# Performance work log

Hardware: AMD Instinct MI355X
Metric: run time of the kernel (lower is better)

## Reference

```python
import jax, jax.numpy as jnp
import numpy as np

EMB = 1024
FF = 4096
NE = 8
TOPK = 2
TEMP = 1.0


def setup_inputs() -> dict:
    key = jax.random.key(0)
    ks = jax.random.split(key, 8)
    s_emb = 1.0 / np.sqrt(EMB)
    s_ff = 1.0 / np.sqrt(FF)
    x = jax.random.normal(ks[0], (4, 2048, EMB), dtype=jnp.float32)
    gate_W = jax.random.uniform(ks[1], (EMB, NE), minval=-s_emb, maxval=s_emb, dtype=jnp.float32)
    gate_b = jax.random.uniform(ks[2], (NE,), minval=-s_emb, maxval=s_emb, dtype=jnp.float32)
    W1 = jax.random.uniform(ks[3], (NE, EMB, FF), minval=-s_emb, maxval=s_emb, dtype=jnp.float32)
    b1 = jax.random.uniform(ks[4], (NE, FF), minval=-s_emb, maxval=s_emb, dtype=jnp.float32)
    W2 = jax.random.uniform(ks[5], (NE, FF, EMB), minval=-s_ff, maxval=s_ff, dtype=jnp.float32)
    b2 = jax.random.uniform(ks[6], (NE, EMB), minval=-s_ff, maxval=s_ff, dtype=jnp.float32)
    return {"x": x, "gate_W": gate_W, "gate_b": gate_b, "W1": W1, "b1": b1, "W2": W2, "b2": b2}


def reference(x, gate_W, gate_b, W1, b1, W2, b2):
    B, S, D = x.shape
    xf = x.reshape(-1, D)  # [T, D]
    T = xf.shape[0]

    gate_logits = (xf @ gate_W + gate_b) / TEMP            # [T, E]
    gate_scores = jax.nn.softmax(gate_logits, axis=-1)     # [T, E]
    topk_scores, topk_idx = jax.lax.top_k(gate_scores, TOPK)
    topk_scores = topk_scores / jnp.sum(topk_scores, axis=-1, keepdims=True)

    # combine_weights[t, e] = sum_i topk_scores[t, i] * (topk_idx[t, i] == e)
    onehot = jax.nn.one_hot(topk_idx, NE, dtype=xf.dtype)  # [T, K, E]
    combine = jnp.einsum('tk,tke->te', topk_scores, onehot)  # [T, E]

    # Dense per-expert FFN (dropout is identity in eval): h = gelu(x W1 + b1); y = h W2 + b2
    h = jax.nn.gelu(jnp.einsum('td,edf->etf', xf, W1) + b1[:, None, :], approximate=False)
    y = jnp.einsum('etf,efd->etd', h, W2) + b2[:, None, :]  # [E, T, D]
    out = jnp.einsum('te,etd->td', combine, y).reshape(B, S, D)

    # Load-balance auxiliary loss
    expert_counts = jnp.sum(onehot, axis=(0, 1))            # [E]
    expert_fraction = expert_counts / (T * TOPK)
    routing_weights = jnp.mean(gate_scores, axis=0)
    aux_loss = NE * jnp.sum(expert_fraction * routing_weights)
    return out, aux_loss
```

## Files before the change

kernel.cpp:

```cpp
#include <hip/hip_runtime.h>
#include <math.h>

#define EMB 1024
#define FF  4096
#define NE  8
#define TTOK 8192

typedef __attribute__((ext_vector_type(4))) float  f32x4;
typedef __attribute__((ext_vector_type(8))) __bf16 bf16x8;
typedef __attribute__((ext_vector_type(4))) __bf16 bf16x4;

#define MAXROWS  18432

#define WS_COUNTS  0
#define WS_CURSORS 1024
#define WS_SSUM    2048
#define WS_CELLB   3072
#define WS_NTILES  4096
#define WS_BASE    4100
#define WS_TILE_E  4160
#define WS_TILE_RB 4800
#define WS_TKIDX   8192
#define WS_TKW     73728
#define WS_SLOT    139264
#define WS_TOKID   204800
#define WS_ROWW    278528
#define WS_BIG2    352256

#define SZ_W1T ((size_t)NE * EMB * FF * 2)
#define SZ_W2T ((size_t)NE * EMB * FF * 2)
#define SZ_XB  ((size_t)TTOK * EMB * 2)
#define SZ_H   ((size_t)MAXROWS * FF * 2)
#define SZ_XG  ((size_t)MAXROWS * EMB * 2)
#define SZ_Y2  ((size_t)MAXROWS * EMB * 2)

__device__ inline f32x4 fzero() { f32x4 v = {0.f, 0.f, 0.f, 0.f}; return v; }

__device__ __forceinline__ void gl16(const void* g, void* l) {
    __builtin_amdgcn_global_load_lds(
        (const __attribute__((address_space(1))) void*)g,
        (__attribute__((address_space(3))) void*)l, 16, 0, 0);
}

#define DSR(dst, addr, off) \
    asm volatile("ds_read_b128 %0, %1 offset:" #off : "=v"(dst) : "v"(addr))

__device__ __forceinline__ float gelu_f(float v) {
    float u = fabsf(v) * 0.70710678118654752f;
    float p = 1.0f + u * (0.278393f + u * (0.230389f + u * (0.000972f + u * 0.078108f)));
    p = p * p; p = p * p;
    float er = 1.0f - 1.0f / p;
    float s = (v >= 0.0f) ? er : -er;
    return 0.5f * v * (1.0f + s);
}

__global__ __launch_bounds__(256) void prepass_kernel(
    const float* __restrict__ W1, __bf16* __restrict__ W1T,
    const float* __restrict__ W2, __bf16* __restrict__ W2T,
    const float* __restrict__ x, const float* __restrict__ gW, const float* __restrict__ gb,
    int* counts, float* ssum, int* tk_idx, float* tk_w, __bf16* __restrict__ xb)
{
    __shared__ __bf16 Ls[64 * 72];
    if (blockIdx.x < 16384) {
        int f = blockIdx.x;
        int which = f >> 13; f &= 8191;
        int e = f >> 10; f &= 1023;
        int R, C, bx, by;
        const float* src; __bf16* dst;
        if (which == 0) { R = EMB; C = FF;  bx = f & 15; by = f >> 4; src = W1; dst = W1T; }
        else            { R = FF;  C = EMB; bx = f & 63; by = f >> 6; src = W2; dst = W2T; }
        src += (size_t)e * R * C;
        dst += (size_t)e * R * C;
        int t = threadIdx.x;
        int r0 = bx * 64, c0 = by * 64;
        int ri = t >> 4, cj = (t & 15) * 4;
#pragma unroll
        for (int p = 0; p < 4; p++) {
            int r = ri + p * 16;
            f32x4 v = *(const f32x4*)(src + (size_t)(r0 + r) * C + c0 + cj);
#pragma unroll
            for (int q = 0; q < 4; q++) Ls[(cj + q) * 72 + r] = (__bf16)v[q];
        }
        __syncthreads();
        int c = t >> 2, rq = (t & 3) * 16;
        bf16x8 a = *(bf16x8*)&Ls[c * 72 + rq];
        bf16x8 b = *(bf16x8*)&Ls[c * 72 + rq + 8];
        *(bf16x8*)(dst + (size_t)(c0 + c) * R + r0 + rq) = a;
        *(bf16x8*)(dst + (size_t)(c0 + c) * R + r0 + rq + 8) = b;
        return;
    }

    int blk = blockIdx.x - 16384;
    int wave = threadIdx.x >> 6;
    int lane = threadIdx.x & 63;
    int t = blk * 4 + wave;

    float acc[NE];
#pragma unroll
    for (int e = 0; e < NE; e++) acc[e] = 0.f;

    const float* xr = x + (size_t)t * EMB;
    __bf16* xbr = xb + (size_t)t * EMB;
#pragma unroll
    for (int i = 0; i < 4; i++) {
        int d0 = i * 256 + lane * 4;
        f32x4 xv = *(const f32x4*)(xr + d0);
        bf16x4 cv;
#pragma unroll
        for (int q = 0; q < 4; q++) cv[q] = (__bf16)xv[q];
        *(bf16x4*)(xbr + d0) = cv;
#pragma unroll
        for (int j = 0; j < 4; j++) {
            const float* wrow = gW + (size_t)(d0 + j) * NE;
            float xs = xv[j];
#pragma unroll
            for (int e = 0; e < NE; e++) acc[e] += xs * wrow[e];
        }
    }
#pragma unroll
    for (int e = 0; e < NE; e++) {
#pragma unroll
        for (int off = 32; off; off >>= 1) acc[e] += __shfl_xor(acc[e], off, 64);
    }
    if (lane == 0) {
        float sc[NE];
        float m = -1e30f;
        for (int e = 0; e < NE; e++) { sc[e] = acc[e] + gb[e]; m = fmaxf(m, sc[e]); }
        float sum = 0.f;
        for (int e = 0; e < NE; e++) { sc[e] = expf(sc[e] - m); sum += sc[e]; }
        float inv = 1.f / sum;
        for (int e = 0; e < NE; e++) sc[e] *= inv;
        int i0 = 0; float s0 = sc[0];
        for (int e = 1; e < NE; e++) if (sc[e] > s0) { s0 = sc[e]; i0 = e; }
        int i1 = -1; float s1 = -1e30f;
        for (int e = 0; e < NE; e++) if (e != i0 && sc[e] > s1) { s1 = sc[e]; i1 = e; }
        float rn = 1.f / (s0 + s1);
        tk_idx[2 * t]     = i0;  tk_idx[2 * t + 1] = i1;
        tk_w[2 * t]       = s0 * rn;  tk_w[2 * t + 1] = s1 * rn;
        int slot = blk & 31;
        atomicAdd(&counts[i0 * 32 + slot], 1);
        atomicAdd(&counts[i1 * 32 + slot], 1);
        for (int e = 0; e < NE; e++) atomicAdd(&ssum[e * 32 + slot], sc[e]);
    }
}

__global__ __launch_bounds__(256) void route_build_kernel(
    const int* counts, const float* ssum,
    int* ntiles, int* base, int* tile_e, int* tile_rb, int* cellbase,
    float* out_aux)
{
    int tid = threadIdx.x;
    int e = tid >> 5, s = tid & 31;
    int c = counts[tid];
    float ss = ssum[tid];

    int inc = c;
#pragma unroll
    for (int d = 1; d < 32; d <<= 1) {
        int t2 = __shfl_up(inc, d, 32);
        if (s >= d) inc += t2;
    }
    float sr = ss;
#pragma unroll
    for (int d = 1; d < 32; d <<= 1) {
        float t2 = __shfl_up(sr, d, 32);
        if (s >= d) sr += t2;
    }

    __shared__ int ctot[NE];
    __shared__ float sstot[NE];
    __shared__ int ebase[NE];
    if (s == 31) { ctot[e] = inc; sstot[e] = sr; }
    __syncthreads();

    if (tid == 0) {
        int total = 0, tiles = 0;
        float aux = 0.f;
        for (int ee = 0; ee < NE; ee++) {
            ebase[ee] = total;
            int nt = (ctot[ee] + 255) >> 8;
            for (int i = 0; i < nt; i++) { tile_e[tiles] = ee; tile_rb[tiles] = total + (i << 8); tiles++; }
            total += nt << 8;
            aux += ((float)ctot[ee] / (float)(TTOK * 2)) * (sstot[ee] / (float)TTOK);
        }
        *ntiles = tiles;
        *out_aux = aux * (float)NE;
    }
    __syncthreads();
    cellbase[tid] = ebase[e] + (inc - c);
    if (s == 0) base[e] = ebase[e];
}

__global__ __launch_bounds__(256) void scatter_kernel(
    const int* __restrict__ tk_idx, const float* __restrict__ tk_w,
    const int* __restrict__ cellbase, int* cursors, int* token_id, float* roww,
    int* slot_of)
{
    int t = blockIdx.x * 256 + threadIdx.x;
    int shard = (t >> 2) & 31;
#pragma unroll
    for (int k = 0; k < 2; k++) {
        int e = tk_idx[2 * t + k];
        int cell = e * 32 + shard;
        int pos = atomicAdd(&cursors[cell], 1);
        int slot = cellbase[cell] + pos;
        token_id[slot] = t;
        roww[slot] = tk_w[2 * t + k];
        slot_of[2 * t + k] = slot;
    }
}

__global__ __launch_bounds__(256) void pack_x_kernel(
    const __bf16* __restrict__ xb, const int* __restrict__ token_id,
    __bf16* __restrict__ xg)
{
    int tid = threadIdx.x;
    int slot = blockIdx.x * 2 + (tid >> 7);
    int off = (tid & 127) * 8;
    int tok = token_id[slot];
    uint4 v = {0u, 0u, 0u, 0u};
    if (tok >= 0) v = *(const uint4*)(xb + (size_t)tok * EMB + off);
    *(uint4*)(xg + (size_t)slot * EMB + off) = v;
}

__global__ __launch_bounds__(256) void combine_kernel(
    const __bf16* __restrict__ y0, const __bf16* __restrict__ y1, int nsplit,
    const int* __restrict__ slot_of,
    const int* __restrict__ tk_idx, const float* __restrict__ tk_w,
    const float* __restrict__ b2, float* __restrict__ out)
{
    int t = blockIdx.x;
    int dq = threadIdx.x * 4;
    int s0 = slot_of[2 * t], s1 = slot_of[2 * t + 1];
    int e0 = tk_idx[2 * t], e1 = tk_idx[2 * t + 1];
    float w0 = tk_w[2 * t], w1 = tk_w[2 * t + 1];
    bf16x4 va = *(const bf16x4*)(y0 + (size_t)s0 * EMB + dq);
    bf16x4 vb = *(const bf16x4*)(y0 + (size_t)s1 * EMB + dq);
    f32x4 ya, yb;
#pragma unroll
    for (int q = 0; q < 4; q++) { ya[q] = (float)va[q]; yb[q] = (float)vb[q]; }
    if (nsplit == 2) {
        bf16x4 za = *(const bf16x4*)(y1 + (size_t)s0 * EMB + dq);
        bf16x4 zb = *(const bf16x4*)(y1 + (size_t)s1 * EMB + dq);
#pragma unroll
        for (int q = 0; q < 4; q++) { ya[q] += (float)za[q]; yb[q] += (float)zb[q]; }
    }
    f32x4 ba = *(const f32x4*)(b2 + (size_t)e0 * EMB + dq);
    f32x4 bb = *(const f32x4*)(b2 + (size_t)e1 * EMB + dq);
    f32x4 r;
#pragma unroll
    for (int q = 0; q < 4; q++) r[q] = w0 * (ya[q] + ba[q]) + w1 * (yb[q] + bb[q]);
    *(f32x4*)(out + (size_t)t * EMB + dq) = r;
}


template <bool PACKED>
__global__ __launch_bounds__(256, 3) void gemm1_8p(
    const __bf16* __restrict__ xsrc, const __bf16* __restrict__ W1T,
    const float* __restrict__ b1,
    const int* __restrict__ token_id, const int* __restrict__ tile_e,
    const int* __restrict__ tile_rb, const int* __restrict__ ntiles,
    __bf16* __restrict__ h)
{
    extern __shared__ __bf16 lds[];
    int flat = blockIdx.x;
    int c8 = flat & 7, r = flat >> 3;
    int nbg = r / 144;
    int rem = r - nbg * 144;
    int sti = rem >> 3;
    int nb  = (nbg << 3) | (rem & 7);
    int st = c8 * 18 + sti;
    if (st >= *ntiles * 2) return;
    int e = tile_e[st >> 1];
    int rb = tile_rb[st >> 1] + (st & 1) * 128;
    int n0 = nb * 128;

    int tid = threadIdx.x, lane = tid & 63, wid = tid >> 6;
    int wr = wid >> 1, wc = wid & 1;
    int cl = lane & 15, cq = lane >> 4;

    int srow1 = ((tid >> 6) << 4) | ((tid & 63) >> 2);
    int schunk = (tid & 3) ^ ((tid >> 3) & 3);
    const __bf16* ag[2];
#pragma unroll
    for (int hm = 0; hm < 2; hm++) {
        int row = srow1 + hm * 64;
        if (PACKED) {
            ag[hm] = xsrc + (size_t)(rb + row) * EMB + schunk * 8;
        } else {
            int tok = token_id[rb + row];
            if (tok < 0) tok = 0;
            ag[hm] = xsrc + (size_t)tok * EMB + schunk * 8;
        }
    }
    const __bf16* bg[2];
#pragma unroll
    for (int hn = 0; hn < 2; hn++)
        bg[hn] = W1T + ((size_t)e * FF + (size_t)(n0 + srow1 + hn * 64)) * EMB + schunk * 8;

    int sdA0 = wid * 512, sdA1 = 2048 + wid * 512;
    int sdB0 = 4096 + wid * 512, sdB1 = 6144 + wid * 512;

    uint32_t lb = (uint32_t)(uintptr_t)(__attribute__((address_space(3))) __bf16*)lds;
    int xoffe = (cq ^ ((cl >> 1) & 3)) * 8;
    uint32_t ab0 = lb + 2u * (uint32_t)(wr * 2048 + cl * 32 + xoffe);
    uint32_t bb0 = lb + 2u * (uint32_t)(4096 + wc * 2048 + cl * 32 + xoffe);

    f32x4 acc[4][4];
#pragma unroll
    for (int i = 0; i < 4; i++)
#pragma unroll
        for (int j = 0; j < 4; j++) acc[i][j] = fzero();

    const int NT = EMB / 32;
#pragma unroll
    for (int t0 = 0; t0 < 2; t0++) {
        __bf16* bp = lds + t0 * 8192;
        int k0 = t0 * 32;
        gl16(ag[0] + k0, bp + sdA0);
        gl16(ag[1] + k0, bp + sdA1);
        gl16(bg[0] + k0, bp + sdB0);
        gl16(bg[1] + k0, bp + sdB1);
    }
    asm volatile("s_waitcnt vmcnt(4)" ::: "memory");
    __builtin_amdgcn_s_barrier();

    int cb = 0;
#pragma unroll 1
    for (int t = 0; t < NT; t++) {
        uint32_t cboff = (uint32_t)cb * 16384u;
        uint32_t aaddr = ab0 + cboff, baddr = bb0 + cboff;
        bf16x8 b[4], a[4];
        DSR(b[0], baddr, 0);    DSR(b[1], baddr, 1024);
        DSR(b[2], baddr, 2048); DSR(b[3], baddr, 3072);
        DSR(a[0], aaddr, 0);    DSR(a[1], aaddr, 1024);
        DSR(a[2], aaddr, 2048); DSR(a[3], aaddr, 3072);

        int kt = t + 2;
        if (kt < NT) {
            int sb = cb + 2; if (sb >= 3) sb -= 3;
            __bf16* sp = lds + sb * 8192;
            int ko = kt * 32;
            gl16(ag[0] + ko, sp + sdA0);
            gl16(ag[1] + ko, sp + sdA1);
            gl16(bg[0] + ko, sp + sdB0);
            gl16(bg[1] + ko, sp + sdB1);
        }

        asm volatile("s_waitcnt lgkmcnt(0)" ::: "memory");
        __builtin_amdgcn_sched_barrier(0);
        __builtin_amdgcn_s_setprio(1);
#pragma unroll
        for (int mi = 0; mi < 4; mi++)
#pragma unroll
            for (int ni = 0; ni < 4; ni++)
                acc[mi][ni] = __builtin_amdgcn_mfma_f32_16x16x32_bf16(a[mi], b[ni], acc[mi][ni], 0, 0, 0);
        __builtin_amdgcn_s_setprio(0);

        if (t < NT - 2)       { asm volatile("s_waitcnt vmcnt(4)" ::: "memory"); }
        else if (t == NT - 2) { asm volatile("s_waitcnt vmcnt(0)" ::: "memory"); }
        if (t < NT - 1) __builtin_amdgcn_s_barrier();
        cb = cb + 1; if (cb >= 3) cb = 0;
    }

    const float* b1g = b1 + (size_t)e * FF + n0;
#pragma unroll
    for (int mi = 0; mi < 4; mi++) {
#pragma unroll
        for (int ni = 0; ni < 4; ni++) {
            int col = wc * 64 + ni * 16 + cl;
            float bias = b1g[col];
#pragma unroll
            for (int j = 0; j < 4; j++) {
                int row = wr * 64 + mi * 16 + cq * 4 + j;
                float v = acc[mi][ni][j] + bias;
                h[(size_t)(rb + row) * FF + n0 + col] = (__bf16)gelu_f(v);
            }
        }
    }
}

__global__ __launch_bounds__(256, 3) void gemm2_128(
    const __bf16* __restrict__ h, const __bf16* __restrict__ W2T,
    const int* __restrict__ tile_e, const int* __restrict__ tile_rb,
    const int* __restrict__ ntiles,
    __bf16* __restrict__ y0, __bf16* __restrict__ y1, int nsplit)
{
    extern __shared__ __bf16 lds[];
    int flat = blockIdx.x;
    int c8 = flat & 7, r = flat >> 3;
    int z = r / 144;
    int rem = r - z * 144;
    int nbg = rem / 72;
    int rem2 = rem - nbg * 72;
    int sti = rem2 >> 2, nbi = rem2 & 3;
    int nb = (nbg << 2) | nbi;
    int st = c8 * 18 + sti;
    if (st >= *ntiles * 2) return;
    int e = tile_e[st >> 1];
    int rb = tile_rb[st >> 1] + (st & 1) * 128;
    int n0 = nb * 128;
    int KC = FF / nsplit;
    int koff = z * KC;
    __bf16* y = z ? y1 : y0;

    int tid = threadIdx.x, lane = tid & 63, wid = tid >> 6;
    int wr = wid >> 1, wc = wid & 1;
    int cl = lane & 15, cq = lane >> 4;

    int srow1 = ((tid >> 6) << 4) | ((tid & 63) >> 2);
    int schunk = (tid & 3) ^ ((tid >> 3) & 3);
    const __bf16* ag[2];
#pragma unroll
    for (int hm = 0; hm < 2; hm++)
        ag[hm] = h + (size_t)(rb + srow1 + hm * 64) * FF + koff + schunk * 8;
    const __bf16* bg[2];
#pragma unroll
    for (int hn = 0; hn < 2; hn++)
        bg[hn] = W2T + ((size_t)e * EMB + (size_t)(n0 + srow1 + hn * 64)) * FF + koff + schunk * 8;

    int sdA0 = wid * 512, sdA1 = 2048 + wid * 512;
    int sdB0 = 4096 + wid * 512, sdB1 = 6144 + wid * 512;

    uint32_t lb = (uint32_t)(uintptr_t)(__attribute__((address_space(3))) __bf16*)lds;
    int xoffe = (cq ^ ((cl >> 1) & 3)) * 8;
    uint32_t ab0 = lb + 2u * (uint32_t)(wr * 2048 + cl * 32 + xoffe);
    uint32_t bb0 = lb + 2u * (uint32_t)(4096 + wc * 2048 + cl * 32 + xoffe);

    f32x4 acc[4][4];
#pragma unroll
    for (int i = 0; i < 4; i++)
#pragma unroll
        for (int j = 0; j < 4; j++) acc[i][j] = fzero();

    const int NT = KC / 32;
#pragma unroll
    for (int t0 = 0; t0 < 2; t0++) {
        __bf16* bp = lds + t0 * 8192;
        int k0 = t0 * 32;
        gl16(ag[0] + k0, bp + sdA0);
        gl16(ag[1] + k0, bp + sdA1);
        gl16(bg[0] + k0, bp + sdB0);
        gl16(bg[1] + k0, bp + sdB1);
    }
    asm volatile("s_waitcnt vmcnt(4)" ::: "memory");
    __builtin_amdgcn_s_barrier();

    int cb = 0;
#pragma unroll 1
    for (int t = 0; t < NT; t++) {
        uint32_t cboff = (uint32_t)cb * 16384u;
        uint32_t aaddr = ab0 + cboff, baddr = bb0 + cboff;
        bf16x8 b[4], a[4];
        DSR(b[0], baddr, 0);    DSR(b[1], baddr, 1024);
        DSR(b[2], baddr, 2048); DSR(b[3], baddr, 3072);
        DSR(a[0], aaddr, 0);    DSR(a[1], aaddr, 1024);
        DSR(a[2], aaddr, 2048); DSR(a[3], aaddr, 3072);

        int kt = t + 2;
        if (kt < NT) {
            int sb = cb + 2; if (sb >= 3) sb -= 3;
            __bf16* sp = lds + sb * 8192;
            int ko = kt * 32;
            gl16(ag[0] + ko, sp + sdA0);
            gl16(ag[1] + ko, sp + sdA1);
            gl16(bg[0] + ko, sp + sdB0);
            gl16(bg[1] + ko, sp + sdB1);
        }

        asm volatile("s_waitcnt lgkmcnt(0)" ::: "memory");
        __builtin_amdgcn_sched_barrier(0);
        __builtin_amdgcn_s_setprio(1);
#pragma unroll
        for (int mi = 0; mi < 4; mi++)
#pragma unroll
            for (int ni = 0; ni < 4; ni++)
                acc[mi][ni] = __builtin_amdgcn_mfma_f32_16x16x32_bf16(a[mi], b[ni], acc[mi][ni], 0, 0, 0);
        __builtin_amdgcn_s_setprio(0);

        if (t < NT - 2)       { asm volatile("s_waitcnt vmcnt(4)" ::: "memory"); }
        else if (t == NT - 2) { asm volatile("s_waitcnt vmcnt(0)" ::: "memory"); }
        if (t < NT - 1) __builtin_amdgcn_s_barrier();
        cb = cb + 1; if (cb >= 3) cb = 0;
    }

#pragma unroll
    for (int mi = 0; mi < 4; mi++) {
#pragma unroll
        for (int ni = 0; ni < 4; ni++) {
            int col = wc * 64 + ni * 16 + cl;
#pragma unroll
            for (int j = 0; j < 4; j++) {
                int row = wr * 64 + mi * 16 + cq * 4 + j;
                y[(size_t)(rb + row) * EMB + n0 + col] = (__bf16)acc[mi][ni][j];
            }
        }
    }
}

extern "C" void kernel_launch(void* const* d_in, const int* in_sizes, int n_in,
                              void* d_out, int out_size, void* d_ws, size_t ws_size,
                              hipStream_t stream)
{
    const float* x   = (const float*)d_in[0];
    const float* gW  = (const float*)d_in[1];
    const float* gb  = (const float*)d_in[2];
    const float* W1  = (const float*)d_in[3];
    const float* b1  = (const float*)d_in[4];
    const float* W2  = (const float*)d_in[5];
    const float* b2  = (const float*)d_in[6];
    float* out = (float*)d_out;

    char* ws = (char*)d_ws;
    int*   counts  = (int*)(ws + WS_COUNTS);
    int*   cursors = (int*)(ws + WS_CURSORS);
    float* ssum    = (float*)(ws + WS_SSUM);
    int*   cellb   = (int*)(ws + WS_CELLB);
    int*   ntiles  = (int*)(ws + WS_NTILES);
    int*   base    = (int*)(ws + WS_BASE);
    int*   tile_e  = (int*)(ws + WS_TILE_E);
    int*   tile_rb = (int*)(ws + WS_TILE_RB);
    int*   tk_idx  = (int*)(ws + WS_TKIDX);
    float* tk_w    = (float*)(ws + WS_TKW);
    int*   slot_of = (int*)(ws + WS_SLOT);
    int*   token_id= (int*)(ws + WS_TOKID);
    float* roww    = (float*)(ws + WS_ROWW);

    __bf16* W1T  = (__bf16*)(ws + WS_BIG2);
    __bf16* xb   = (__bf16*)(ws + WS_BIG2 + SZ_W1T);
    __bf16* W2T  = (__bf16*)(ws + WS_BIG2 + SZ_W1T + SZ_XB);
    __bf16* hbuf = (__bf16*)(ws + WS_BIG2 + SZ_W1T + SZ_XB + SZ_W2T);
    size_t fixedend = WS_BIG2 + SZ_W1T + SZ_XB + SZ_W2T;

    __bf16* y0 = (__bf16*)(ws + WS_BIG2);
    __bf16* xg = (__bf16*)(ws + fixedend + SZ_H);
    bool packed = (ws_size >= fixedend + SZ_H + SZ_XG);
    __bf16* y1 = (__bf16*)(ws + fixedend + SZ_H + (packed ? SZ_XG : 0));
    int nsplit = (ws_size >= fixedend + SZ_H + (packed ? SZ_XG : 0) + SZ_Y2) ? 2 : 1;

    hipFuncSetAttribute((const void*)gemm1_8p<true>,  hipFuncAttributeMaxDynamicSharedMemorySize, 49152);
    hipFuncSetAttribute((const void*)gemm1_8p<false>, hipFuncAttributeMaxDynamicSharedMemorySize, 49152);
    hipFuncSetAttribute((const void*)gemm2_128, hipFuncAttributeMaxDynamicSharedMemorySize, 49152);

    hipMemsetAsync(ws + WS_COUNTS, 0, 3072, stream);
    hipMemsetAsync(ws + WS_TOKID, 0xFF, (size_t)MAXROWS * 4, stream);

    prepass_kernel<<<16384 + TTOK / 4, 256, 0, stream>>>(
        W1, W1T, W2, W2T, x, gW, gb, counts, ssum, tk_idx, tk_w, xb);
    route_build_kernel<<<1, 256, 0, stream>>>(counts, ssum, ntiles, base, tile_e, tile_rb,
                                              cellb, out + (size_t)TTOK * EMB);
    scatter_kernel<<<TTOK / 256, 256, 0, stream>>>(tk_idx, tk_w, cellb, cursors, token_id, roww, slot_of);

    if (packed) {
        pack_x_kernel<<<MAXROWS / 2, 256, 0, stream>>>(xb, token_id, xg);
        gemm1_8p<true><<<8 * 18 * 32, 256, 49152, stream>>>(
            xg, W1T, b1, token_id, tile_e, tile_rb, ntiles, hbuf);
    } else {
        gemm1_8p<false><<<8 * 18 * 32, 256, 49152, stream>>>(
            xb, W1T, b1, token_id, tile_e, tile_rb, ntiles, hbuf);
    }
    gemm2_128<<<8 * 144 * nsplit, 256, 49152, stream>>>(
        hbuf, W2T, tile_e, tile_rb, ntiles, y0, y1, nsplit);
    combine_kernel<<<TTOK, 256, 0, stream>>>(y0, y1, nsplit, slot_of, tk_idx, tk_w, b2, out);
}
```

Measured before the change: 610.7 us.

## Switch GEMM pipelines to double buffering and raise occupancy to five blocks

Both grouped GEMM kernels move from a three-stage LDS ring to a two-buffer scheme, cutting dynamic shared memory from 48KB to 32KB per block. Launch bounds are raised to allow five blocks per CU, aiming to hide memory latency through more resident waves. The trade-off is shallower prefetch with a full vmcnt(0) wait each iteration, plus possible register pressure or spills from the tighter occupancy target.

Result: slower. 1.329 ms (+117.7%).

```diff
diff --git a/kernel.cpp b/kernel.cpp
--- a/kernel.cpp
+++ b/kernel.cpp
@@ -255,7 +255,7 @@
 
 
 template <bool PACKED>
-__global__ __launch_bounds__(256, 3) void gemm1_8p(
+__global__ __launch_bounds__(256, 5) void gemm1_8p(
     const __bf16* __restrict__ xsrc, const __bf16* __restrict__ W1T,
     const float* __restrict__ b1,
     const int* __restrict__ token_id, const int* __restrict__ tile_e,
@@ -313,22 +313,26 @@
         for (int j = 0; j < 4; j++) acc[i][j] = fzero();
 
     const int NT = EMB / 32;
-#pragma unroll
-    for (int t0 = 0; t0 < 2; t0++) {
-        __bf16* bp = lds + t0 * 8192;
-        int k0 = t0 * 32;
-        gl16(ag[0] + k0, bp + sdA0);
-        gl16(ag[1] + k0, bp + sdA1);
-        gl16(bg[0] + k0, bp + sdB0);
-        gl16(bg[1] + k0, bp + sdB1);
-    }
-    asm volatile("s_waitcnt vmcnt(4)" ::: "memory");
+    gl16(ag[0], lds + sdA0);
+    gl16(ag[1], lds + sdA1);
+    gl16(bg[0], lds + sdB0);
+    gl16(bg[1], lds + sdB1);
+    asm volatile("s_waitcnt vmcnt(0)" ::: "memory");
     __builtin_amdgcn_s_barrier();
 
-    int cb = 0;
 #pragma unroll 1
     for (int t = 0; t < NT; t++) {
-        uint32_t cboff = (uint32_t)cb * 16384u;
+        int kt = t + 1;
+        if (kt < NT) {
+            __bf16* sp = lds + (kt & 1) * 8192;
+            int ko = kt * 32;
+            gl16(ag[0] + ko, sp + sdA0);
+            gl16(ag[1] + ko, sp + sdA1);
+            gl16(bg[0] + ko, sp + sdB0);
+            gl16(bg[1] + ko, sp + sdB1);
+        }
+
+        uint32_t cboff = (uint32_t)(t & 1) * 16384u;
         uint32_t aaddr = ab0 + cboff, baddr = bb0 + cboff;
         bf16x8 b[4], a[4];
         DSR(b[0], baddr, 0);    DSR(b[1], baddr, 1024);
@@ -336,17 +340,6 @@
         DSR(a[0], aaddr, 0);    DSR(a[1], aaddr, 1024);
         DSR(a[2], aaddr, 2048); DSR(a[3], aaddr, 3072);
 
-        int kt = t + 2;
-        if (kt < NT) {
-            int sb = cb + 2; if (sb >= 3) sb -= 3;
-            __bf16* sp = lds + sb * 8192;
-            int ko = kt * 32;
-            gl16(ag[0] + ko, sp + sdA0);
-            gl16(ag[1] + ko, sp + sdA1);
-            gl16(bg[0] + ko, sp + sdB0);
-            gl16(bg[1] + ko, sp + sdB1);
-        }
-
         asm volatile("s_waitcnt lgkmcnt(0)" ::: "memory");
         __builtin_amdgcn_sched_barrier(0);
         __builtin_amdgcn_s_setprio(1);
@@ -357,10 +350,8 @@
                 acc[mi][ni] = __builtin_amdgcn_mfma_f32_16x16x32_bf16(a[mi], b[ni], acc[mi][ni], 0, 0, 0);
         __builtin_amdgcn_s_setprio(0);
 
-        if (t < NT - 2)       { asm volatile("s_waitcnt vmcnt(4)" ::: "memory"); }
-        else if (t == NT - 2) { asm volatile("s_waitcnt vmcnt(0)" ::: "memory"); }
+        asm volatile("s_waitcnt vmcnt(0)" ::: "memory");
         if (t < NT - 1) __builtin_amdgcn_s_barrier();
-        cb = cb + 1; if (cb >= 3) cb = 0;
     }
 
     const float* b1g = b1 + (size_t)e * FF + n0;
@@ -380,7 +371,7 @@
     }
 }
 
-__global__ __launch_bounds__(256, 3) void gemm2_128(
+__global__ __launch_bounds__(256, 5) void gemm2_128(
     const __bf16* __restrict__ h, const __bf16* __restrict__ W2T,
     const int* __restrict__ tile_e, const int* __restrict__ tile_rb,
     const int* __restrict__ ntiles,
@@ -434,22 +425,26 @@
         for (int j = 0; j < 4; j++) acc[i][j] = fzero();
 
     const int NT = KC / 32;
-#pragma unroll
-    for (int t0 = 0; t0 < 2; t0++) {
-        __bf16* bp = lds + t0 * 8192;
-        int k0 = t0 * 32;
-        gl16(ag[0] + k0, bp + sdA0);
-        gl16(ag[1] + k0, bp + sdA1);
-        gl16(bg[0] + k0, bp + sdB0);
-        gl16(bg[1] + k0, bp + sdB1);
-    }
-    asm volatile("s_waitcnt vmcnt(4)" ::: "memory");
+    gl16(ag[0], lds + sdA0);
+    gl16(ag[1], lds + sdA1);
+    gl16(bg[0], lds + sdB0);
+    gl16(bg[1], lds + sdB1);
+    asm volatile("s_waitcnt vmcnt(0)" ::: "memory");
     __builtin_amdgcn_s_barrier();
 
-    int cb = 0;
 #pragma unroll 1
     for (int t = 0; t < NT; t++) {
-        uint32_t cboff = (uint32_t)cb * 16384u;
+        int kt = t + 1;
+        if (kt < NT) {
+            __bf16* sp = lds + (kt & 1) * 8192;
+            int ko = kt * 32;
+            gl16(ag[0] + ko, sp + sdA0);
+            gl16(ag[1] + ko, sp + sdA1);
+            gl16(bg[0] + ko, sp + sdB0);
+            gl16(bg[1] + ko, sp + sdB1);
+        }
+
+        uint32_t cboff = (uint32_t)(t & 1) * 16384u;
         uint32_t aaddr = ab0 + cboff, baddr = bb0 + cboff;
         bf16x8 b[4], a[4];
         DSR(b[0], baddr, 0);    DSR(b[1], baddr, 1024);
@@ -457,17 +452,6 @@
         DSR(a[0], aaddr, 0);    DSR(a[1], aaddr, 1024);
         DSR(a[2], aaddr, 2048); DSR(a[3], aaddr, 3072);
 
-        int kt = t + 2;
-        if (kt < NT) {
-            int sb = cb + 2; if (sb >= 3) sb -= 3;
-            __bf16* sp = lds + sb * 8192;
-            int ko = kt * 32;
-            gl16(ag[0] + ko, sp + sdA0);
-            gl16(ag[1] + ko, sp + sdA1);
-            gl16(bg[0] + ko, sp + sdB0);
-            gl16(bg[1] + ko, sp + sdB1);
-        }
-
         asm volatile("s_waitcnt lgkmcnt(0)" ::: "memory");
         __builtin_amdgcn_sched_barrier(0);
         __builtin_amdgcn_s_setprio(1);
@@ -478,10 +462,8 @@
                 acc[mi][ni] = __builtin_amdgcn_mfma_f32_16x16x32_bf16(a[mi], b[ni], acc[mi][ni], 0, 0, 0);
         __builtin_amdgcn_s_setprio(0);
 
-        if (t < NT - 2)       { asm volatile("s_waitcnt vmcnt(4)" ::: "memory"); }
-        else if (t == NT - 2) { asm volatile("s_waitcnt vmcnt(0)" ::: "memory"); }
+        asm volatile("s_waitcnt vmcnt(0)" ::: "memory");
         if (t < NT - 1) __builtin_amdgcn_s_barrier();
-        cb = cb + 1; if (cb >= 3) cb = 0;
     }
 
 #pragma unroll
@@ -538,9 +520,9 @@
     __bf16* y1 = (__bf16*)(ws + fixedend + SZ_H + (packed ? SZ_XG : 0));
     int nsplit = (ws_size >= fixedend + SZ_H + (packed ? SZ_XG : 0) + SZ_Y2) ? 2 : 1;
 
-    hipFuncSetAttribute((const void*)gemm1_8p<true>,  hipFuncAttributeMaxDynamicSharedMemorySize, 49152);
-    hipFuncSetAttribute((const void*)gemm1_8p<false>, hipFuncAttributeMaxDynamicSharedMemorySize, 49152);
-    hipFuncSetAttribute((const void*)gemm2_128, hipFuncAttributeMaxDynamicSharedMemorySize, 49152);
+    hipFuncSetAttribute((const void*)gemm1_8p<true>,  hipFuncAttributeMaxDynamicSharedMemorySize, 32768);
+    hipFuncSetAttribute((const void*)gemm1_8p<false>, hipFuncAttributeMaxDynamicSharedMemorySize, 32768);
+    hipFuncSetAttribute((const void*)gemm2_128, hipFuncAttributeMaxDynamicSharedMemorySize, 32768);
 
     hipMemsetAsync(ws + WS_COUNTS, 0, 3072, stream);
     hipMemsetAsync(ws + WS_TOKID, 0xFF, (size_t)MAXROWS * 4, stream);
@@ -553,13 +535,13 @@
 
     if (packed) {
         pack_x_kernel<<<MAXROWS / 2, 256, 0, stream>>>(xb, token_id, xg);
-        gemm1_8p<true><<<8 * 18 * 32, 256, 49152, stream>>>(
+        gemm1_8p<true><<<8 * 18 * 32, 256, 32768, stream>>>(
             xg, W1T, b1, token_id, tile_e, tile_rb, ntiles, hbuf);
     } else {
-        gemm1_8p<false><<<8 * 18 * 32, 256, 49152, stream>>>(
+        gemm1_8p<false><<<8 * 18 * 32, 256, 32768, stream>>>(
             xb, W1T, b1, token_id, tile_e, tile_rb, ntiles, hbuf);
     }
-    gemm2_128<<<8 * 144 * nsplit, 256, 49152, stream>>>(
+    gemm2_128<<<8 * 144 * nsplit, 256, 32768, stream>>>(
         hbuf, W2T, tile_e, tile_rb, ntiles, y0, y1, nsplit);
     combine_kernel<<<TTOK, 256, 0, stream>>>(y0, y1, nsplit, slot_of, tk_idx, tk_w, b2, out);
 }
```
